# Kernel tuning notes

Measured on AMD Instinct MI355X. Metric: run time of the kernel, lower is better.

## Reference

```python
import jax, jax.numpy as jnp
import numpy as np

N_NODES = 50000
N_EDGES = 1600000
N_GRAPHS = 64
DIM_IN, DIM_H, HEADS, DIM_OUT = 128, 32, 2, 64
NEG_SLOPE = 0.2


def _segment_softmax(scores, seg, num_segments):
    # scores: [E, H], seg: [E] int -> softmax over edges sharing the same dst
    m = jax.ops.segment_max(scores, seg, num_segments=num_segments)
    m = jnp.where(jnp.isfinite(m), m, 0.0)  # empty segments -> -inf; neutralize
    e = jnp.exp(scores - m[seg])
    s = jax.ops.segment_sum(e, seg, num_segments=num_segments)
    return e / (s[seg] + 1e-16)


def gatv2_conv(x, edge_index, Wl, Wr, att, bias, heads, ch, n_nodes):
    # PyG GATv2Conv defaults: add_self_loops=True, share_weights=False, concat heads.
    loops = jnp.arange(n_nodes, dtype=edge_index.dtype)
    ei = jnp.concatenate([edge_index, jnp.stack([loops, loops])], axis=1)
    src, dst = ei[0], ei[1]
    xl = (x @ Wl).reshape(n_nodes, heads, ch)  # source transform
    xr = (x @ Wr).reshape(n_nodes, heads, ch)  # target transform
    el = xl[src]                               # [E+N, H, C] gather
    s = jax.nn.leaky_relu(el + xr[dst], NEG_SLOPE)
    scores = jnp.einsum('ehc,hc->eh', s, att)  # [E+N, H]
    alpha = _segment_softmax(scores, dst, n_nodes)
    out = jax.ops.segment_sum(alpha[..., None] * el, dst, num_segments=n_nodes)
    return out.reshape(n_nodes, heads * ch) + bias


def setup_inputs() -> dict:
    key = jax.random.key(0)
    ks = jax.random.split(key, 12)
    glorot = lambda k, shp: jax.random.normal(k, shp, jnp.float32) * np.sqrt(2.0 / (shp[0] + shp[-1]))
    x = jax.random.normal(ks[0], (N_NODES, DIM_IN), jnp.float32)
    edge_index = jax.random.randint(ks[1], (2, N_EDGES), 0, N_NODES, jnp.int64)
    batch = jnp.sort(jax.random.randint(ks[2], (N_NODES,), 0, N_GRAPHS, jnp.int64))
    H1 = DIM_H * HEADS
    return {
        'x': x, 'edge_index': edge_index, 'batch': batch,
        'Wl1': glorot(ks[3], (DIM_IN, H1)), 'Wr1': glorot(ks[4], (DIM_IN, H1)),
        'att1': glorot(ks[5], (HEADS, DIM_H)), 'b1': jnp.zeros((H1,), jnp.float32),
        'Wl2': glorot(ks[6], (H1, DIM_OUT)), 'Wr2': glorot(ks[7], (H1, DIM_OUT)),
        'att2': glorot(ks[8], (1, DIM_OUT)), 'b2': jnp.zeros((DIM_OUT,), jnp.float32),
        'lin_w': glorot(ks[9], (DIM_OUT, 2)), 'lin_b': jnp.zeros((2,), jnp.float32),
    }


def reference(x, edge_index, batch, Wl1, Wr1, att1, b1, Wl2, Wr2, att2, b2, lin_w, lin_b):
    # eval mode: dropout is identity
    h = gatv2_conv(x, edge_index, Wl1, Wr1, att1, b1, HEADS, DIM_H, N_NODES)
    h = jax.nn.elu(h)
    h = jax.nn.elu(gatv2_conv(h, edge_index, Wl2, Wr2, att2, b2, 1, DIM_OUT, N_NODES))
    # global mean pool over graphs
    sums = jax.ops.segment_sum(h, batch, num_segments=N_GRAPHS)
    cnts = jax.ops.segment_sum(jnp.ones((N_NODES,), h.dtype), batch, num_segments=N_GRAPHS)
    pooled = sums / jnp.maximum(cnts, 1.0)[:, None]
    return pooled @ lin_w + lin_b
```

## Files before the change

kernel.cpp:

```cpp
#include <hip/hip_runtime.h>
#include <hip/hip_bf16.h>
#include <math.h>

#define N_NODES 50000
#define N_EDGES 1600000
#define N_GRAPHS 64
#define NB 391
#define NBLK 256
#define CHUNK 6250
#define ROW_STRIDE 80
#define SENT 50047

typedef unsigned int u32;
typedef __attribute__((ext_vector_type(8))) __bf16 bf16x8;
typedef __attribute__((ext_vector_type(4))) float f32x4;

__device__ __forceinline__ float bcf(u32 u) { return __builtin_bit_cast(float, u); }

template <int CTRL>
__device__ __forceinline__ float dpp_add(float v) {
    int r = __builtin_amdgcn_update_dpp(0, __builtin_bit_cast(int, v), CTRL, 0xF, 0xF, true);
    return v + __builtin_bit_cast(float, r);
}

__device__ __forceinline__ u32 pack_bf16x2(float lo, float hi) {
    unsigned short l = __builtin_bit_cast(unsigned short, __float2bfloat16(lo));
    unsigned short h = __builtin_bit_cast(unsigned short, __float2bfloat16(hi));
    return (u32)l | ((u32)h << 16);
}

template <int K>
__global__ __launch_bounds__(256) void conv_w(
    const float* __restrict__ Wl, const float* __restrict__ Wr,
    u32* __restrict__ wfHi, u32* __restrict__ wfLo) {
    const int KO = K / 32;
    for (int idx = threadIdx.x; idx < KO * 8 * 64; idx += 256) {
        const int L = idx & 63;
        const int tile = idx >> 6;
        const int ko = tile >> 3, nt = tile & 7;
        const int c = nt * 16 + (L & 15);
        u32 hi[4], lo[4];
        float hv[8], lv[8];
#pragma unroll
        for (int i = 0; i < 8; ++i) {
            const int k = ko * 32 + (L >> 4) * 8 + i;
            const float wv = (c < 64) ? Wl[k * 64 + c] : Wr[k * 64 + (c - 64)];
            const __hip_bfloat16 h = __float2bfloat16(wv);
            hv[i] = wv;
            lv[i] = wv - __bfloat162float(h);
        }
#pragma unroll
        for (int i = 0; i < 4; ++i) {
            hi[i] = pack_bf16x2(hv[2 * i], hv[2 * i + 1]);
            lo[i] = pack_bf16x2(lv[2 * i], lv[2 * i + 1]);
        }
        *(uint4*)(wfHi + (size_t)idx * 4) = make_uint4(hi[0], hi[1], hi[2], hi[3]);
        *(uint4*)(wfLo + (size_t)idx * 4) = make_uint4(lo[0], lo[1], lo[2], lo[3]);
    }
}

__global__ __launch_bounds__(256) void conv_x_count(
    const float* __restrict__ x, u32* __restrict__ xbf,
    const int* __restrict__ ei, int* __restrict__ countsRM, int convBlocks) {
    __shared__ int h[NB];
    if (blockIdx.x >= convBlocks) {
        const int t = threadIdx.x;
        const int cb = blockIdx.x - convBlocks;
        for (int k = t; k < NB; k += 256) h[k] = 0;
        __syncthreads();
        const int base = cb * CHUNK;
        for (int e = base + t; e < base + CHUNK; e += 256)
            atomicAdd(&h[ei[N_EDGES + e] >> 7], 1);
        __syncthreads();
        for (int k = t; k < NB; k += 256) countsRM[cb * NB + k] = h[k];
        return;
    }
    const int units = N_NODES * 128 / 8;
    const int stride = convBlocks * 256;
    for (int u = blockIdx.x * 256 + threadIdx.x; u < units; u += stride) {
        const float4 a = *(const float4*)(x + (size_t)u * 8);
        const float4 b = *(const float4*)(x + (size_t)u * 8 + 4);
        *(uint4*)(xbf + (size_t)u * 4) = make_uint4(
            pack_bf16x2(a.x, a.y), pack_bf16x2(a.z, a.w),
            pack_bf16x2(b.x, b.y), pack_bf16x2(b.z, b.w));
    }
}

__global__ __launch_bounds__(256) void scan_bucket(
    const int* __restrict__ countsRM, int* __restrict__ scanT,
    int* __restrict__ totals) {
    __shared__ int tmp[256];
    const int b = blockIdx.x;
    const int t = threadIdx.x;
    const int v0 = countsRM[t * NB + b];
    tmp[t] = v0;
    __syncthreads();
    for (int off = 1; off < 256; off <<= 1) {
        int v = (t >= off) ? tmp[t - off] : 0;
        __syncthreads();
        tmp[t] += v;
        __syncthreads();
    }
    scanT[b * 256 + t] = tmp[t] - v0;
    if (t == 255) totals[b] = tmp[t];
}

__global__ __launch_bounds__(512) void scan_total(
    const int* __restrict__ totals, int* __restrict__ bucketBase,
    float* __restrict__ alb) {
    __shared__ int tmp[512];
    const int t = threadIdx.x;
    const int v0 = (t < NB) ? totals[t] : 0;
    tmp[t] = v0;
    __syncthreads();
    for (int off = 1; off < 512; off <<= 1) {
        int v = (t >= off) ? tmp[t - off] : 0;
        __syncthreads();
        tmp[t] += v;
        __syncthreads();
    }
    if (t < NB) bucketBase[t] = tmp[t] - v0;
    if (t == NB - 1) bucketBase[NB] = tmp[t];
    if (t == 0) { alb[(size_t)SENT * 2] = -1e30f; alb[(size_t)SENT * 2 + 1] = -1e30f; }
}

template <int K, bool FUSE_SCATTER>
__global__ __launch_bounds__(256) void gemm_mfma(
    const u32* __restrict__ xbf, const u32* __restrict__ wfHi,
    const u32* __restrict__ wfLo, const float* __restrict__ att,
    u32* __restrict__ xlb, float* __restrict__ xr,
    float* __restrict__ alb, float* __restrict__ arb,
    const int* __restrict__ ei, const int* __restrict__ scanT,
    const int* __restrict__ bb, int* __restrict__ sortedE, int gemmBlocks) {
    __shared__ float Ct[64][129];
    __shared__ float alq[64][4];
    const int t = threadIdx.x;
    if (FUSE_SCATTER && blockIdx.x >= gemmBlocks) {
        int* cursor = (int*)&Ct[0][0];
        const int b = blockIdx.x - gemmBlocks;
        for (int k = t; k < NB; k += 256)
            cursor[k] = bb[k] + scanT[k * 256 + b];
        __syncthreads();
        const int base = b * CHUNK;
        for (int e = base + t; e < base + CHUNK; e += 256) {
            const int s = ei[e];
            const int d = ei[N_EDGES + e];
            const int idx = atomicAdd(&cursor[d >> 7], 1);
            sortedE[idx] = (s << 7) | (d & 127);
        }
        return;
    }
    const int KO = K / 32;
    const int lane = t & 63;
    const int w = __builtin_amdgcn_readfirstlane(t >> 6);
    const int quad = lane >> 4;
    const int m16 = lane & 15;
    const int base = blockIdx.x * 64;
    const int arow = base + w * 16 + m16;
    const u32* aptr = xbf + ((size_t)arow * K + quad * 8) / 2;

    f32x4 acc[8];
    const f32x4 zz = {0.f, 0.f, 0.f, 0.f};
#pragma unroll
    for (int i = 0; i < 8; ++i) acc[i] = zz;

#pragma unroll
    for (int ko = 0; ko < KO; ++ko) {
        const uint4 au = *(const uint4*)(aptr + ko * 16);
        const bf16x8 af = __builtin_bit_cast(bf16x8, au);
#pragma unroll
        for (int nt = 0; nt < 8; ++nt) {
            const uint4 bh = *(const uint4*)(wfHi + (size_t)((ko * 8 + nt) * 64 + lane) * 4);
            acc[nt] = __builtin_amdgcn_mfma_f32_16x16x32_bf16(
                af, __builtin_bit_cast(bf16x8, bh), acc[nt], 0, 0, 0);
        }
#pragma unroll
        for (int nt = 0; nt < 8; ++nt) {
            const uint4 bl = *(const uint4*)(wfLo + (size_t)((ko * 8 + nt) * 64 + lane) * 4);
            acc[nt] = __builtin_amdgcn_mfma_f32_16x16x32_bf16(
                af, __builtin_bit_cast(bf16x8, bl), acc[nt], 0, 0, 0);
        }
    }
#pragma unroll
    for (int nt = 0; nt < 8; ++nt)
#pragma unroll
        for (int r = 0; r < 4; ++r)
            Ct[w * 16 + quad * 4 + r][nt * 16 + m16] = acc[nt][r];
    __syncthreads();

    const int node = t & 63;
    const int q = t >> 6;
    const int n = base + node;
    float av = 0.f;
    if (n < N_NODES) {
        if (q < 2) {
            u32 pk[16];
#pragma unroll
            for (int j = 0; j < 32; j += 2) {
                const float v0 = Ct[node][q * 32 + j];
                const float v1 = Ct[node][q * 32 + j + 1];
                av = fmaf(att[q * 32 + j], v0, av);
                av = fmaf(att[q * 32 + j + 1], v1, av);
                pk[j >> 1] = pack_bf16x2(v0, v1);
            }
            uint4* dst = (uint4*)(xlb + (size_t)n * 32 + q * 16);
#pragma unroll
            for (int j = 0; j < 4; ++j)
                dst[j] = make_uint4(pk[j * 4], pk[j * 4 + 1], pk[j * 4 + 2], pk[j * 4 + 3]);
        } else {
            const int cb = (q - 2) * 32;
#pragma unroll
            for (int j = 0; j < 32; j += 4) {
                float4 v = {Ct[node][64 + cb + j], Ct[node][64 + cb + j + 1],
                            Ct[node][64 + cb + j + 2], Ct[node][64 + cb + j + 3]};
                av = fmaf(att[cb + j], v.x, av);
                av = fmaf(att[cb + j + 1], v.y, av);
                av = fmaf(att[cb + j + 2], v.z, av);
                av = fmaf(att[cb + j + 3], v.w, av);
                *(float4*)(xr + (size_t)n * 64 + cb + j) = v;
            }
        }
    }
    alq[node][q] = av;
    __syncthreads();
    if (t < 64 && base + t < N_NODES) {
        const int nn = base + t;
        if (K == 128) {
            alb[(size_t)nn * 2] = alq[t][0];
            alb[(size_t)nn * 2 + 1] = alq[t][1];
        } else {
            alb[nn] = alq[t][0] + alq[t][1];
        }
        arb[(size_t)nn * 2] = alq[t][2];
        arb[(size_t)nn * 2 + 1] = alq[t][3];
    }
    if (K == 64 && blockIdx.x == 0 && t == 0) alb[SENT] = -1e30f;
}

__global__ __launch_bounds__(256) void expand_kernel(
    const int* __restrict__ bucketBase, const int* __restrict__ sortedE,
    int* __restrict__ deg, int* __restrict__ rows) {
    __shared__ int ldeg[128];
    const int b = blockIdx.x;
    const int t = threadIdx.x;
    const int node_base = b * 128;
    if (t < 128) {
        const int n = node_base + t;
        ldeg[t] = 1;
        if (n < N_NODES) rows[(size_t)n * ROW_STRIDE] = n;
    }
    __syncthreads();
    const int beg = bucketBase[b];
    const int end = bucketBase[b + 1];
    for (int i = beg + t; i < end; i += 256) {
        const int en = sortedE[i];
        const int ld = en & 127;
        const int pos = atomicAdd(&ldeg[ld], 1);
        if (pos < ROW_STRIDE) rows[(size_t)(node_base + ld) * ROW_STRIDE + pos] = en >> 7;
    }
    __syncthreads();
    if (t < 128) {
        const int n = node_base + t;
        if (n < N_NODES) {
            int c = ldeg[t];
            c = c < ROW_STRIDE ? c : ROW_STRIDE;
            const int cp = (c + 7) & ~7;
            for (int j = c; j < cp; ++j) rows[(size_t)n * ROW_STRIDE + j] = SENT;
            deg[n] = cp;
        }
    }
}

template <bool L1>
__global__ __launch_bounds__(256) void node_layer(
    const int* __restrict__ deg, const int* __restrict__ rows,
    const u32* __restrict__ xlb, const float* __restrict__ xr,
    const float* __restrict__ alb, const float* __restrict__ arb,
    const float* __restrict__ att, const float* __restrict__ bias,
    u32* __restrict__ houtB, float* __restrict__ houtF) {
    const int n = (blockIdx.x * 256 + threadIdx.x) >> 6;
    const int lane = threadIdx.x & 63;
    const int sub = lane & 7;
    const int g = lane >> 3;
    const float4 xra = *(const float4*)(xr + (size_t)n * 64 + sub * 8);
    const float4 xrb = *(const float4*)(xr + (size_t)n * 64 + sub * 8 + 4);
    const float4 ata = *(const float4*)(att + sub * 8);
    const float4 atb = *(const float4*)(att + sub * 8 + 4);
    const float2 ar2 = *(const float2*)(arb + (size_t)n * 2);
    const float based = 0.6f * (L1 ? ((sub & 4) ? ar2.y : ar2.x) : (ar2.x + ar2.y));

    float c0 = 0.f, c1 = 0.f, c2 = 0.f, c3 = 0.f;
    float c4 = 0.f, c5 = 0.f, c6 = 0.f, c7 = 0.f;
    float ssum = 0.f;
    const int cp = __builtin_amdgcn_readfirstlane(deg[n]);
    const int* __restrict__ row = rows + (size_t)n * ROW_STRIDE;
    for (int i = 0; i < cp; i += 8) {
        const int s = row[i + g];
        const float als = L1 ? alb[(size_t)s * 2 + ((sub >> 2) & 1)] : alb[s];
        const uint4 r4 = *(const uint4*)(xlb + (size_t)s * 32 + sub * 4);
        const float a0 = bcf(r4.x << 16), a1 = bcf(r4.x & 0xFFFF0000u);
        const float a2f = bcf(r4.y << 16), a3 = bcf(r4.y & 0xFFFF0000u);
        const float a4 = bcf(r4.z << 16), a5 = bcf(r4.z & 0xFFFF0000u);
        const float a6 = bcf(r4.w << 16), a7 = bcf(r4.w & 0xFFFF0000u);
        float v = ata.x * fabsf(a0 + xra.x);
        v = fmaf(ata.y, fabsf(a1 + xra.y), v);
        v = fmaf(ata.z, fabsf(a2f + xra.z), v);
        v = fmaf(ata.w, fabsf(a3 + xra.w), v);
        v = fmaf(atb.x, fabsf(a4 + xrb.x), v);
        v = fmaf(atb.y, fabsf(a5 + xrb.y), v);
        v = fmaf(atb.z, fabsf(a6 + xrb.z), v);
        v = fmaf(atb.w, fabsf(a7 + xrb.w), v);
        v = dpp_add<0xB1>(v);
        v = dpp_add<0x4E>(v);
        if (!L1) v = dpp_add<0x141>(v);
        const float ev = __expf(fmaf(0.6f, als, fmaf(0.4f, v, based)));
        c0 = fmaf(ev, a0, c0); c1 = fmaf(ev, a1, c1);
        c2 = fmaf(ev, a2f, c2); c3 = fmaf(ev, a3, c3);
        c4 = fmaf(ev, a4, c4); c5 = fmaf(ev, a5, c5);
        c6 = fmaf(ev, a6, c6); c7 = fmaf(ev, a7, c7);
        ssum += ev;
    }
#define XRED(x) x += __shfl_xor(x, 8); x += __shfl_xor(x, 16); x += __shfl_xor(x, 32);
    XRED(c0) XRED(c1) XRED(c2) XRED(c3) XRED(c4) XRED(c5) XRED(c6) XRED(c7) XRED(ssum)
#undef XRED
    if (g == 0) {
        const float inv = 1.f / (ssum + 1e-16f);
        const float4 ba = *(const float4*)(bias + sub * 8);
        const float4 bb = *(const float4*)(bias + sub * 8 + 4);
        float o[8] = {c0 * inv + ba.x, c1 * inv + ba.y, c2 * inv + ba.z, c3 * inv + ba.w,
                      c4 * inv + bb.x, c5 * inv + bb.y, c6 * inv + bb.z, c7 * inv + bb.w};
#pragma unroll
        for (int j = 0; j < 8; ++j) o[j] = o[j] > 0.f ? o[j] : expm1f(o[j]);
        if (L1) {
            *(uint4*)(houtB + (size_t)n * 32 + sub * 4) = make_uint4(
                pack_bf16x2(o[0], o[1]), pack_bf16x2(o[2], o[3]),
                pack_bf16x2(o[4], o[5]), pack_bf16x2(o[6], o[7]));
        } else {
            *(float4*)(houtF + (size_t)n * 64 + sub * 8) = make_float4(o[0], o[1], o[2], o[3]);
            *(float4*)(houtF + (size_t)n * 64 + sub * 8 + 4) = make_float4(o[4], o[5], o[6], o[7]);
        }
    }
}

__global__ __launch_bounds__(64) void pool_kernel(
    const float* __restrict__ h2, const int* __restrict__ batch,
    float* __restrict__ pooled, float* __restrict__ cnt) {
    const int t = threadIdx.x;
    const int base = blockIdx.x * 64;
    float local = 0.f, lc = 0.f;
    int cur = -1;
    for (int j = 0; j < 64; ++j) {
        const int n = base + j;
        if (n >= N_NODES) break;
        const int g = batch[n];
        if (g != cur) {
            if (cur >= 0) {
                unsafeAtomicAdd(&pooled[cur * 64 + t], local);
                if (t == 0) unsafeAtomicAdd(&cnt[cur], lc);
            }
            cur = g; local = 0.f; lc = 0.f;
        }
        local += h2[n * 64 + t];
        lc += 1.f;
    }
    if (cur >= 0) {
        unsafeAtomicAdd(&pooled[cur * 64 + t], local);
        if (t == 0) unsafeAtomicAdd(&cnt[cur], lc);
    }
}

__global__ __launch_bounds__(128) void head_kernel(
    const float* __restrict__ pooled, const float* __restrict__ cnt,
    const float* __restrict__ lin_w, const float* __restrict__ lin_b,
    float* __restrict__ out) {
    const int i = threadIdx.x;
    const int g = i >> 1, k = i & 1;
    float c = cnt[g];
    c = c > 1.f ? c : 1.f;
    float a = 0.f;
#pragma unroll
    for (int j = 0; j < 64; ++j) a = fmaf(pooled[g * 64 + j] / c, lin_w[j * 2 + k], a);
    out[i] = a + lin_b[k];
}

extern "C" void kernel_launch(void* const* d_in, const int* in_sizes, int n_in,
                              void* d_out, int out_size, void* d_ws, size_t ws_size,
                              hipStream_t stream) {
    const float* x     = (const float*)d_in[0];
    const int*   ei    = (const int*)d_in[1];
    const int*   batch = (const int*)d_in[2];
    const float* Wl1   = (const float*)d_in[3];
    const float* Wr1   = (const float*)d_in[4];
    const float* att1  = (const float*)d_in[5];
    const float* b1    = (const float*)d_in[6];
    const float* Wl2   = (const float*)d_in[7];
    const float* Wr2   = (const float*)d_in[8];
    const float* att2  = (const float*)d_in[9];
    const float* b2    = (const float*)d_in[10];
    const float* lin_w = (const float*)d_in[11];
    const float* lin_b = (const float*)d_in[12];

    float* ws = (float*)d_ws;
    u32*   xbf      = (u32*)ws;
    u32*   h1b      = (u32*)(ws + 3203072);
    u32*   xlb      = (u32*)(ws + 4804608);
    float* xr       = ws + 6406144;
    float* h2       = ws + 9609216;
    float* alb      = ws + 12812288;
    float* arb      = ws + 12912384;
    int*   rows     = (int*)(ws + 13012480);
    int*   deg      = (int*)(ws + 17016320);
    int*   countsRM = (int*)(ws + 17066368);
    int*   scanT    = (int*)(ws + 17166464);
    int*   totals   = (int*)(ws + 17266560);
    int*   bb       = (int*)(ws + 17267072);
    float* pooled   = ws + 17267584;
    float* cnt      = ws + 17271680;
    int*   sortedE  = (int*)(ws + 17271744);
    u32*   wf1hi    = (u32*)(ws + 18871744);
    u32*   wf1lo    = (u32*)(ws + 18879936);
    u32*   wf2hi    = (u32*)(ws + 18888128);
    u32*   wf2lo    = (u32*)(ws + 18892224);

    hipMemsetAsync(pooled, 0, (size_t)(4096 + 64) * sizeof(float), stream);

    const int gblocks = (N_NODES + 63) / 64;
    const int convBlocks = 512;

    conv_w<128><<<1, 256, 0, stream>>>(Wl1, Wr1, wf1hi, wf1lo);
    conv_w<64><<<1, 256, 0, stream>>>(Wl2, Wr2, wf2hi, wf2lo);
    conv_x_count<<<convBlocks + NBLK, 256, 0, stream>>>(x, xbf, ei, countsRM, convBlocks);

    scan_bucket<<<NB, 256, 0, stream>>>(countsRM, scanT, totals);
    scan_total<<<1, 512, 0, stream>>>(totals, bb, alb);

    gemm_mfma<128, true><<<gblocks + NBLK, 256, 0, stream>>>(
        xbf, wf1hi, wf1lo, att1, xlb, xr, alb, arb, ei, scanT, bb, sortedE, gblocks);

    expand_kernel<<<NB, 256, 0, stream>>>(bb, sortedE, deg, rows);

    node_layer<true><<<N_NODES / 4, 256, 0, stream>>>(
        deg, rows, xlb, xr, alb, arb, att1, b1, h1b, nullptr);

    gemm_mfma<64, false><<<gblocks, 256, 0, stream>>>(
        h1b, wf2hi, wf2lo, att2, xlb, xr, alb, arb, nullptr, nullptr, nullptr, nullptr, gblocks);
    node_layer<false><<<N_NODES / 4, 256, 0, stream>>>(
        deg, rows, xlb, xr, alb, arb, att2, b2, nullptr, h2);

    pool_kernel<<<(N_NODES + 63) / 64, 64, 0, stream>>>(h2, batch, pooled, cnt);
    head_kernel<<<1, 128, 0, stream>>>(pooled, cnt, lin_w, lin_b, (float*)d_out);
}
```

Before: 297.8 us.

## Fuse preprocessing kernels, convert x in GEMM, and merge pool with head

Weight conversion, bucket counting and both scan stages now run in one kernel. The last block to finish, found through an atomic counter, does the scans serially. The separate x-to-bf16 conversion pass is removed, and the first GEMM reads fp32 x directly and packs it to bf16 in registers. Pooling and the linear head are merged with the same last-block pattern. This cuts the launch count from 11 to 6 and drops a full read/write pass over x, at the cost of a serial scan done by a single block.

```diff
diff --git a/kernel.cpp b/kernel.cpp
--- a/kernel.cpp
+++ b/kernel.cpp
@@ -29,9 +29,8 @@
     return (u32)l | ((u32)h << 16);
 }
 
-template <int K>
-__global__ __launch_bounds__(256) void conv_w(
-    const float* __restrict__ Wl, const float* __restrict__ Wr,
+__device__ __forceinline__ void conv_w_dev(
+    int K, const float* __restrict__ Wl, const float* __restrict__ Wr,
     u32* __restrict__ wfHi, u32* __restrict__ wfLo) {
     const int KO = K / 32;
     for (int idx = threadIdx.x; idx < KO * 8 * 64; idx += 256) {
@@ -59,75 +58,55 @@
     }
 }
 
-__global__ __launch_bounds__(256) void conv_x_count(
-    const float* __restrict__ x, u32* __restrict__ xbf,
-    const int* __restrict__ ei, int* __restrict__ countsRM, int convBlocks) {
+__global__ __launch_bounds__(256) void build0(
+    const int* __restrict__ ei,
+    const float* __restrict__ Wl1, const float* __restrict__ Wr1,
+    const float* __restrict__ Wl2, const float* __restrict__ Wr2,
+    u32* __restrict__ wf1hi, u32* __restrict__ wf1lo,
+    u32* __restrict__ wf2hi, u32* __restrict__ wf2lo,
+    int* __restrict__ countsCM, int* __restrict__ scanT,
+    int* __restrict__ bb, float* __restrict__ alb, int* __restrict__ done) {
+    const int t = threadIdx.x;
+    if (blockIdx.x == 256) { conv_w_dev(128, Wl1, Wr1, wf1hi, wf1lo); return; }
+    if (blockIdx.x == 257) { conv_w_dev(64, Wl2, Wr2, wf2hi, wf2lo); return; }
     __shared__ int h[NB];
-    if (blockIdx.x >= convBlocks) {
-        const int t = threadIdx.x;
-        const int cb = blockIdx.x - convBlocks;
-        for (int k = t; k < NB; k += 256) h[k] = 0;
-        __syncthreads();
-        const int base = cb * CHUNK;
-        for (int e = base + t; e < base + CHUNK; e += 256)
-            atomicAdd(&h[ei[N_EDGES + e] >> 7], 1);
-        __syncthreads();
-        for (int k = t; k < NB; k += 256) countsRM[cb * NB + k] = h[k];
-        return;
-    }
-    const int units = N_NODES * 128 / 8;
-    const int stride = convBlocks * 256;
-    for (int u = blockIdx.x * 256 + threadIdx.x; u < units; u += stride) {
-        const float4 a = *(const float4*)(x + (size_t)u * 8);
-        const float4 b = *(const float4*)(x + (size_t)u * 8 + 4);
-        *(uint4*)(xbf + (size_t)u * 4) = make_uint4(
-            pack_bf16x2(a.x, a.y), pack_bf16x2(a.z, a.w),
-            pack_bf16x2(b.x, b.y), pack_bf16x2(b.z, b.w));
-    }
-}
-
-__global__ __launch_bounds__(256) void scan_bucket(
-    const int* __restrict__ countsRM, int* __restrict__ scanT,
-    int* __restrict__ totals) {
-    __shared__ int tmp[256];
-    const int b = blockIdx.x;
-    const int t = threadIdx.x;
-    const int v0 = countsRM[t * NB + b];
-    tmp[t] = v0;
-    __syncthreads();
-    for (int off = 1; off < 256; off <<= 1) {
-        int v = (t >= off) ? tmp[t - off] : 0;
-        __syncthreads();
-        tmp[t] += v;
-        __syncthreads();
-    }
-    scanT[b * 256 + t] = tmp[t] - v0;
-    if (t == 255) totals[b] = tmp[t];
-}
-
-__global__ __launch_bounds__(512) void scan_total(
-    const int* __restrict__ totals, int* __restrict__ bucketBase,
-    float* __restrict__ alb) {
-    __shared__ int tmp[512];
-    const int t = threadIdx.x;
-    const int v0 = (t < NB) ? totals[t] : 0;
-    tmp[t] = v0;
-    __syncthreads();
-    for (int off = 1; off < 512; off <<= 1) {
-        int v = (t >= off) ? tmp[t - off] : 0;
-        __syncthreads();
-        tmp[t] += v;
-        __syncthreads();
-    }
-    if (t < NB) bucketBase[t] = tmp[t] - v0;
-    if (t == NB - 1) bucketBase[NB] = tmp[t];
-    if (t == 0) { alb[(size_t)SENT * 2] = -1e30f; alb[(size_t)SENT * 2 + 1] = -1e30f; }
-}
-
-template <int K, bool FUSE_SCATTER>
+    __shared__ int lastFlag;
+    const int cb = blockIdx.x;
+    for (int k = t; k < NB; k += 256) h[k] = 0;
+    __syncthreads();
+    const int base = cb * CHUNK;
+    for (int e = base + t; e < base + CHUNK; e += 256)
+        atomicAdd(&h[ei[N_EDGES + e] >> 7], 1);
+    __syncthreads();
+    for (int k = t; k < NB; k += 256) countsCM[k * 256 + cb] = h[k];
+    __threadfence();
+    if (t == 0) lastFlag = (atomicAdd(done, 1) == NBLK - 1);
+    __syncthreads();
+    if (!lastFlag) return;
+    __threadfence();
+    __shared__ int totals[NB];
+    for (int b = t; b < NB; b += 256) {
+        int run = 0;
+        const int* src = countsCM + b * 256;
+        int* dst = scanT + b * 256;
+        for (int i = 0; i < 256; ++i) { dst[i] = run; run += src[i]; }
+        totals[b] = run;
+    }
+    __syncthreads();
+    if (t == 0) {
+        int run = 0;
+        for (int k = 0; k < NB; ++k) { bb[k] = run; run += totals[k]; }
+        bb[NB] = run;
+        alb[(size_t)SENT * 2] = -1e30f;
+        alb[(size_t)SENT * 2 + 1] = -1e30f;
+    }
+}
+
+template <int K, bool AF32, bool FUSE_SCATTER>
 __global__ __launch_bounds__(256) void gemm_mfma(
-    const u32* __restrict__ xbf, const u32* __restrict__ wfHi,
-    const u32* __restrict__ wfLo, const float* __restrict__ att,
+    const float* __restrict__ xF, const u32* __restrict__ xB,
+    const u32* __restrict__ wfHi, const u32* __restrict__ wfLo,
+    const float* __restrict__ att,
     u32* __restrict__ xlb, float* __restrict__ xr,
     float* __restrict__ alb, float* __restrict__ arb,
     const int* __restrict__ ei, const int* __restrict__ scanT,
@@ -157,7 +136,7 @@
     const int m16 = lane & 15;
     const int base = blockIdx.x * 64;
     const int arow = base + w * 16 + m16;
-    const u32* aptr = xbf + ((size_t)arow * K + quad * 8) / 2;
+    const int rowc = arow < N_NODES ? arow : N_NODES - 1;
 
     f32x4 acc[8];
     const f32x4 zz = {0.f, 0.f, 0.f, 0.f};
@@ -166,8 +145,18 @@
 
 #pragma unroll
     for (int ko = 0; ko < KO; ++ko) {
-        const uint4 au = *(const uint4*)(aptr + ko * 16);
-        const bf16x8 af = __builtin_bit_cast(bf16x8, au);
+        bf16x8 af;
+        if (AF32) {
+            const float* ap = xF + (size_t)rowc * K + ko * 32 + quad * 8;
+            const float4 a0 = *(const float4*)ap;
+            const float4 a1 = *(const float4*)(ap + 4);
+            af = __builtin_bit_cast(bf16x8, make_uint4(
+                pack_bf16x2(a0.x, a0.y), pack_bf16x2(a0.z, a0.w),
+                pack_bf16x2(a1.x, a1.y), pack_bf16x2(a1.z, a1.w)));
+        } else {
+            af = __builtin_bit_cast(bf16x8,
+                *(const uint4*)(xB + ((size_t)rowc * K + ko * 32 + quad * 8) / 2));
+        }
 #pragma unroll
         for (int nt = 0; nt < 8; ++nt) {
             const uint4 bh = *(const uint4*)(wfHi + (size_t)((ko * 8 + nt) * 64 + lane) * 4);
@@ -342,9 +331,12 @@
     }
 }
 
-__global__ __launch_bounds__(64) void pool_kernel(
+__global__ __launch_bounds__(64) void pool_head(
     const float* __restrict__ h2, const int* __restrict__ batch,
-    float* __restrict__ pooled, float* __restrict__ cnt) {
+    float* __restrict__ pooled, float* __restrict__ cnt,
+    const float* __restrict__ lin_w, const float* __restrict__ lin_b,
+    float* __restrict__ out, int* __restrict__ done2, int nblocks) {
+    __shared__ int lastFlag;
     const int t = threadIdx.x;
     const int base = blockIdx.x * 64;
     float local = 0.f, lc = 0.f;
@@ -367,20 +359,22 @@
         unsafeAtomicAdd(&pooled[cur * 64 + t], local);
         if (t == 0) unsafeAtomicAdd(&cnt[cur], lc);
     }
-}
-
-__global__ __launch_bounds__(128) void head_kernel(
-    const float* __restrict__ pooled, const float* __restrict__ cnt,
-    const float* __restrict__ lin_w, const float* __restrict__ lin_b,
-    float* __restrict__ out) {
-    const int i = threadIdx.x;
-    const int g = i >> 1, k = i & 1;
-    float c = cnt[g];
-    c = c > 1.f ? c : 1.f;
-    float a = 0.f;
-#pragma unroll
-    for (int j = 0; j < 64; ++j) a = fmaf(pooled[g * 64 + j] / c, lin_w[j * 2 + k], a);
-    out[i] = a + lin_b[k];
+    __threadfence();
+    if (t == 0) lastFlag = (atomicAdd(done2, 1) == nblocks - 1);
+    __syncthreads();
+    if (!lastFlag) return;
+    __threadfence();
+#pragma unroll
+    for (int rep = 0; rep < 2; ++rep) {
+        const int i = rep * 64 + t;
+        const int g = i >> 1, k = i & 1;
+        float c = cnt[g];
+        c = c > 1.f ? c : 1.f;
+        float a = 0.f;
+#pragma unroll
+        for (int j = 0; j < 64; ++j) a = fmaf(pooled[g * 64 + j] / c, lin_w[j * 2 + k], a);
+        out[i] = a + lin_b[k];
+    }
 }
 
 extern "C" void kernel_launch(void* const* d_in, const int* in_sizes, int n_in,
@@ -401,52 +395,51 @@
     const float* lin_b = (const float*)d_in[12];
 
     float* ws = (float*)d_ws;
-    u32*   xbf      = (u32*)ws;
-    u32*   h1b      = (u32*)(ws + 3203072);
-    u32*   xlb      = (u32*)(ws + 4804608);
-    float* xr       = ws + 6406144;
-    float* h2       = ws + 9609216;
-    float* alb      = ws + 12812288;
-    float* arb      = ws + 12912384;
-    int*   rows     = (int*)(ws + 13012480);
-    int*   deg      = (int*)(ws + 17016320);
-    int*   countsRM = (int*)(ws + 17066368);
-    int*   scanT    = (int*)(ws + 17166464);
-    int*   totals   = (int*)(ws + 17266560);
-    int*   bb       = (int*)(ws + 17267072);
-    float* pooled   = ws + 17267584;
-    float* cnt      = ws + 17271680;
-    int*   sortedE  = (int*)(ws + 17271744);
-    u32*   wf1hi    = (u32*)(ws + 18871744);
-    u32*   wf1lo    = (u32*)(ws + 18879936);
-    u32*   wf2hi    = (u32*)(ws + 18888128);
-    u32*   wf2lo    = (u32*)(ws + 18892224);
-
-    hipMemsetAsync(pooled, 0, (size_t)(4096 + 64) * sizeof(float), stream);
+    u32*   h1b      = (u32*)ws;
+    u32*   xlb      = (u32*)(ws + 1601536);
+    float* xr       = ws + 3203072;
+    float* h2       = ws + 6406144;
+    float* alb      = ws + 9609216;
+    float* arb      = ws + 9709312;
+    int*   rows     = (int*)(ws + 9809408);
+    int*   deg      = (int*)(ws + 13813248);
+    int*   countsCM = (int*)(ws + 13863296);
+    int*   scanT    = (int*)(ws + 13963392);
+    int*   bb       = (int*)(ws + 14063488);
+    int*   sortedE  = (int*)(ws + 14064000);
+    u32*   wf1hi    = (u32*)(ws + 15664000);
+    u32*   wf1lo    = (u32*)(ws + 15672192);
+    u32*   wf2hi    = (u32*)(ws + 15680384);
+    u32*   wf2lo    = (u32*)(ws + 15684480);
+    float* pooled   = ws + 15688576;
+    float* cnt      = ws + 15692672;
+    int*   done     = (int*)(ws + 15692736);
+    int*   done2    = (int*)(ws + 15692737);
+
+    hipMemsetAsync(pooled, 0, (size_t)(4096 + 64 + 2) * sizeof(float), stream);
 
     const int gblocks = (N_NODES + 63) / 64;
-    const int convBlocks = 512;
-
-    conv_w<128><<<1, 256, 0, stream>>>(Wl1, Wr1, wf1hi, wf1lo);
-    conv_w<64><<<1, 256, 0, stream>>>(Wl2, Wr2, wf2hi, wf2lo);
-    conv_x_count<<<convBlocks + NBLK, 256, 0, stream>>>(x, xbf, ei, countsRM, convBlocks);
-
-    scan_bucket<<<NB, 256, 0, stream>>>(countsRM, scanT, totals);
-    scan_total<<<1, 512, 0, stream>>>(totals, bb, alb);
-
-    gemm_mfma<128, true><<<gblocks + NBLK, 256, 0, stream>>>(
-        xbf, wf1hi, wf1lo, att1, xlb, xr, alb, arb, ei, scanT, bb, sortedE, gblocks);
+
+    build0<<<NBLK + 2, 256, 0, stream>>>(
+        ei, Wl1, Wr1, Wl2, Wr2, wf1hi, wf1lo, wf2hi, wf2lo,
+        countsCM, scanT, bb, alb, done);
+
+    gemm_mfma<128, true, true><<<gblocks + NBLK, 256, 0, stream>>>(
+        x, nullptr, wf1hi, wf1lo, att1, xlb, xr, alb, arb,
+        ei, scanT, bb, sortedE, gblocks);
 
     expand_kernel<<<NB, 256, 0, stream>>>(bb, sortedE, deg, rows);
 
     node_layer<true><<<N_NODES / 4, 256, 0, stream>>>(
         deg, rows, xlb, xr, alb, arb, att1, b1, h1b, nullptr);
 
-    gemm_mfma<64, false><<<gblocks, 256, 0, stream>>>(
-        h1b, wf2hi, wf2lo, att2, xlb, xr, alb, arb, nullptr, nullptr, nullptr, nullptr, gblocks);
+    gemm_mfma<64, false, false><<<gblocks, 256, 0, stream>>>(
+        nullptr, h1b, wf2hi, wf2lo, att2, xlb, xr, alb, arb,
+        nullptr, nullptr, nullptr, nullptr, gblocks);
     node_layer<false><<<N_NODES / 4, 256, 0, stream>>>(
         deg, rows, xlb, xr, alb, arb, att2, b2, nullptr, h2);
 
-    pool_kernel<<<(N_NODES + 63) / 64, 64, 0, stream>>>(h2, batch, pooled, cnt);
-    head_kernel<<<1, 128, 0, stream>>>(pooled, cnt, lin_w, lin_b, (float*)d_out);
-}
+    const int pblocks = (N_NODES + 63) / 64;
+    pool_head<<<pblocks, 64, 0, stream>>>(
+        h2, batch, pooled, cnt, lin_w, lin_b, (float*)d_out, done2, pblocks);
+}
```

Result: slower. 375.5 us (+26.1%).
